# Performance work log

Measured on AMD Instinct MI355X. Metric: run time of the kernel, lower is better.

## Reference

```python
import jax, jax.numpy as jnp
import numpy as np

N = 32768
D = 512          # query_dim = key_dim = value_dim
H = 8            # num_heads


def setup_inputs() -> dict:
    key = jax.random.key(0)
    ks = jax.random.split(key, 8)
    s = 0.02
    return {
        "queries": jax.random.normal(ks[0], (N, D), dtype=jnp.float32),
        "keys": jax.random.normal(ks[1], (N, D), dtype=jnp.float32),
        "values": jax.random.normal(ks[2], (N, D), dtype=jnp.float32),
        # Linear weights stored as [in, out] (torch stores [out, in]; math identical)
        "Wq": jax.random.normal(ks[3], (D, D * H), dtype=jnp.float32) * s,
        "Wk": jax.random.normal(ks[4], (D, D * H), dtype=jnp.float32) * s,
        "Wv": jax.random.normal(ks[5], (D, D * H), dtype=jnp.float32) * s,
        "Wo": jax.random.normal(ks[6], (D * H, D), dtype=jnp.float32) * s,
        "bo": jax.random.normal(ks[7], (D,), dtype=jnp.float32) * s,
    }


def reference(queries, keys, values, Wq, Wk, Wv, Wo, bo):
    # Projections: [N, D] -> [N, H, D]
    Q = (queries @ Wq).reshape(-1, H, D)
    K = (keys @ Wk).reshape(-1, H, D)
    V = (values @ Wv).reshape(-1, H, D)
    # Per-token attention across the HEADS axis (faithful to torch.bmm on [N,H,D])
    attn = jnp.einsum("nhd,ngd->nhg", Q, K)      # [N, H, H], no 1/sqrt(d) scaling
    attn = jax.nn.softmax(attn, axis=-1)
    out = jnp.einsum("nhg,ngd->nhd", attn, V)    # [N, H, D]
    out = out.reshape(-1, H * D)
    return out @ Wo + bo                           # [N, D]
```

## Files before the change

### kernel.cpp

```cpp
#include <hip/hip_runtime.h>
#include <hip/hip_bf16.h>
#include <cstdint>


typedef unsigned short u16;
typedef unsigned int u32;
typedef __bf16 bf16x8 __attribute__((ext_vector_type(8)));
typedef float f32x4 __attribute__((ext_vector_type(4)));

#define DEVI __device__ __forceinline__

DEVI float b2f(u16 u) {
    union { u32 i; float f; } c; c.i = ((u32)u) << 16; return c.f;
}
DEVI u16 f2b(float f) {
    union { float f; u32 i; } c; c.f = f;
    return (u16)((c.i + 0x7FFFu + ((c.i >> 16) & 1u)) >> 16);
}
DEVI float asf(u32 x) { union { u32 i; float f; } c; c.i = x; return c.f; }

DEVI void async16(const u16* g, u16* l) {
    __builtin_amdgcn_global_load_lds(
        (const __attribute__((address_space(1))) u32*)g,
        (__attribute__((address_space(3))) u32*)l, 16, 0, 0);
}


__global__ __launch_bounds__(256) void cvt3_bf16(
    const float* __restrict__ a, const float* __restrict__ b,
    const float* __restrict__ c, u16* __restrict__ out, long ostride) {
    const float* in = (blockIdx.z == 0) ? a : (blockIdx.z == 1) ? b : c;
    u16* o = out + (long)blockIdx.z * ostride;
    const int i = blockIdx.x * 256 + threadIdx.x;
    const float4 x = ((const float4*)in)[2 * i];
    const float4 y = ((const float4*)in)[2 * i + 1];
    union { u16 u[8]; uint4 v; } r;
    r.u[0] = f2b(x.x); r.u[1] = f2b(x.y); r.u[2] = f2b(x.z); r.u[3] = f2b(x.w);
    r.u[4] = f2b(y.x); r.u[5] = f2b(y.y); r.u[6] = f2b(y.z); r.u[7] = f2b(y.w);
    ((uint4*)o)[i] = r.v;
}

__global__ void transpose_cvt(const float* __restrict__ in, u16* __restrict__ out,
                              int R, int C) {
    __shared__ float tile[32][33];
    const int c0 = blockIdx.x * 32, r0 = blockIdx.y * 32;
    const int x = threadIdx.x, y = threadIdx.y;
#pragma unroll
    for (int i = 0; i < 4; ++i) {
        const int r = y + i * 8;
        tile[x][r] = in[(long)(r0 + r) * C + c0 + x];
    }
    __syncthreads();
#pragma unroll
    for (int i = 0; i < 4; ++i) {
        const int c = y + i * 8;
        out[(long)(c0 + c) * R + r0 + x] = f2b(tile[c][x]);
    }
}


#define VM4 asm volatile("s_waitcnt vmcnt(4)" ::: "memory")
#define VM0 asm volatile("s_waitcnt vmcnt(0)" ::: "memory")
#define LGKM0 asm volatile("s_waitcnt lgkmcnt(0)" ::: "memory")
#define NOOP ((void)0)

#define STAGE_A(t, h)                                                     \
    do {                                                                  \
        const u16* _s = pA + (long)(h) * 128 * K + (long)(t) * 64;        \
        u16* _d = As + (((t) & 1) * 16384) + (h) * 8192 + wave * 512;     \
        async16(_s, _d);                                                  \
        async16(_s + 64 * (long)K, _d + 4096);                            \
    } while (0)

#define STAGE_B(t, h)                                                     \
    do {                                                                  \
        const u16* _s = pB + (long)(h) * 128 * K + (long)(t) * 64;        \
        u16* _d = Bs + (((t) & 1) * 16384) + (h) * 8192 + wave * 512;     \
        async16(_s, _d);                                                  \
        async16(_s + 64 * (long)K, _d + 4096);                            \
    } while (0)

#define PHASE(c, P, STG, VW)                                                   \
    {                                                                          \
        const u16* _sA = As + (c) * 16384;                                     \
        const u16* _sB = Bs + (c) * 16384;                                     \
        bf16x8 a00 = *(const bf16x8*)(_sA + arow_u + (2 * (P)) * 1024 + s0);   \
        bf16x8 a01 = *(const bf16x8*)(_sA + arow_u + (2 * (P)) * 1024 + s1);   \
        bf16x8 a10 = *(const bf16x8*)(_sA + arow_u + (2 * (P) + 1) * 1024 + s0); \
        bf16x8 a11 = *(const bf16x8*)(_sA + arow_u + (2 * (P) + 1) * 1024 + s1); \
        if ((P) == 0) {                                                        \
            _Pragma("unroll") for (int n = 0; n < 4; ++n) {                    \
                bfr[n][0] = *(const bf16x8*)(_sB + brow_u + n * 1024 + s0);    \
                bfr[n][1] = *(const bf16x8*)(_sB + brow_u + n * 1024 + s1);    \
            }                                                                  \
        }                                                                      \
        STG;                                                                   \
        __builtin_amdgcn_s_barrier();                                          \
        LGKM0;                                                                 \
        __builtin_amdgcn_s_setprio(1);                                         \
        _Pragma("unroll") for (int n = 0; n < 4; ++n) {                        \
            acc[2 * (P)][n] = __builtin_amdgcn_mfma_f32_16x16x32_bf16(         \
                a00, bfr[n][0], acc[2 * (P)][n], 0, 0, 0);                     \
            acc[2 * (P)][n] = __builtin_amdgcn_mfma_f32_16x16x32_bf16(         \
                a01, bfr[n][1], acc[2 * (P)][n], 0, 0, 0);                     \
            acc[2 * (P) + 1][n] = __builtin_amdgcn_mfma_f32_16x16x32_bf16(     \
                a10, bfr[n][0], acc[2 * (P) + 1][n], 0, 0, 0);                 \
            acc[2 * (P) + 1][n] = __builtin_amdgcn_mfma_f32_16x16x32_bf16(     \
                a11, bfr[n][1], acc[2 * (P) + 1][n], 0, 0, 0);                 \
        }                                                                      \
        __builtin_amdgcn_s_setprio(0);                                         \
        VW;                                                                    \
        __builtin_amdgcn_s_barrier();                                          \
    }

template <int F32OUT>
__global__ __launch_bounds__(512, 2) void gemm256(
    const u16* __restrict__ Ab, const u16* __restrict__ Bb,
    void* __restrict__ Cv, const float* __restrict__ bias,
    int M, int N, int K, long sAz, long sBz, long sCz) {
    __shared__ u16 As[2 * 16384];
    __shared__ u16 Bs[2 * 16384];
    (void)M;
    const int tid = threadIdx.x;
    const int wave = tid >> 6, lane = tid & 63;
    const int z = blockIdx.z;
    const u16* A = Ab + (long)z * sAz;
    const u16* BT = Bb + (long)z * sBz;

    int bx, by;
    {
        const int gx = gridDim.x, nwg = gx * gridDim.y;
        const int b = blockIdx.y * gx + blockIdx.x;
        if ((nwg & 7) == 0) {
            const int cpx = nwg >> 3;
            const int w = (b & 7) * cpx + (b >> 3);
            bx = w % gx; by = w / gx;
        } else { bx = blockIdx.x; by = blockIdx.y; }
    }
    const long row0 = (long)by * 256, col0 = (long)bx * 256;

    const int mrow = lane & 15, quad = lane >> 4;
    const int wr = wave >> 2, wc = wave & 3;
    const int s0 = ((quad ^ (mrow & 7)) << 3);
    const int s1 = (((4 | quad) ^ (mrow & 7)) << 3);
    const int arow_u = (wr * 128 + mrow) * 64;
    const int brow_u = (wc * 64 + mrow) * 64;

    const int sr = tid >> 3;
    const int skg = ((tid & 7) ^ (sr & 7)) << 3;
    const u16* pA = A + (row0 + sr) * (long)K + skg;
    const u16* pB = BT + (col0 + sr) * (long)K + skg;

    f32x4 acc[8][4] = {};
    bf16x8 bfr[4][2];

    const int NT = K >> 6;
    const int NI = NT >> 1;

    STAGE_A(0, 0); STAGE_A(0, 1); STAGE_B(0, 0); STAGE_B(0, 1);
    STAGE_B(1, 0); STAGE_B(1, 1);
    VM4;
    __builtin_amdgcn_s_barrier();

#pragma unroll 1
    for (int it = 0; it < NI - 1; ++it) {
        const int t1 = 2 * it + 1;
        PHASE(0, 0, STAGE_A(t1, 0), NOOP);
        PHASE(0, 1, STAGE_A(t1, 1), NOOP);
        PHASE(0, 2, STAGE_B(t1 + 1, 0), NOOP);
        PHASE(0, 3, STAGE_B(t1 + 1, 1), VM4);
        PHASE(1, 0, STAGE_A(t1 + 1, 0), NOOP);
        PHASE(1, 1, STAGE_A(t1 + 1, 1), NOOP);
        PHASE(1, 2, STAGE_B(t1 + 2, 0), NOOP);
        PHASE(1, 3, STAGE_B(t1 + 2, 1), VM4);
    }
    {
        const int tl = NT - 1;
        PHASE(0, 0, STAGE_A(tl, 0), NOOP);
        PHASE(0, 1, STAGE_A(tl, 1), NOOP);
        PHASE(0, 2, NOOP, NOOP);
        PHASE(0, 3, NOOP, VM0);
        PHASE(1, 0, NOOP, NOOP);
        PHASE(1, 1, NOOP, NOOP);
        PHASE(1, 2, NOOP, NOOP);
        PHASE(1, 3, NOOP, NOOP);
    }

    const long wrow = row0 + wr * 128;
    const long wcol = col0 + wc * 64;
    if (F32OUT) {
        float* C = (float*)Cv + (long)z * sCz;
        float bv[4];
#pragma unroll
        for (int n = 0; n < 4; ++n) bv[n] = bias[wcol + n * 16 + mrow];
#pragma unroll
        for (int m = 0; m < 8; ++m) {
            const long r = wrow + m * 16 + quad * 4;
#pragma unroll
            for (int n = 0; n < 4; ++n) {
                const long c = wcol + n * 16 + mrow;
#pragma unroll
                for (int rr = 0; rr < 4; ++rr)
                    C[(r + rr) * (long)N + c] = acc[m][n][rr] + bv[n];
            }
        }
    } else {
        u16* C = (u16*)Cv + (long)z * sCz;
#pragma unroll
        for (int m = 0; m < 8; ++m) {
            const long r = wrow + m * 16 + quad * 4;
#pragma unroll
            for (int n = 0; n < 4; ++n) {
                const long c = wcol + n * 16 + mrow;
#pragma unroll
                for (int rr = 0; rr < 4; ++rr)
                    C[(r + rr) * (long)N + c] = f2b(acc[m][n][rr]);
            }
        }
    }
}

#undef PHASE
#undef STAGE_A
#undef STAGE_B


DEVI float dot8(uint4 a, uint4 b) {
    const u32* pa = (const u32*)&a;
    const u32* pb = (const u32*)&b;
    float s = 0.f;
#pragma unroll
    for (int w = 0; w < 4; ++w) {
        s = fmaf(asf(pa[w] << 16), asf(pb[w] << 16), s);
        s = fmaf(asf(pa[w] & 0xFFFF0000u), asf(pb[w] & 0xFFFF0000u), s);
    }
    return s;
}

DEVI void acc8(float* o, uint4 v, float p) {
    const u32* pv = (const u32*)&v;
#pragma unroll
    for (int w = 0; w < 4; ++w) {
        o[2 * w]     = fmaf(p, asf(pv[w] << 16), o[2 * w]);
        o[2 * w + 1] = fmaf(p, asf(pv[w] & 0xFFFF0000u), o[2 * w + 1]);
    }
}

__global__ __launch_bounds__(256) void attn_kernel(
    const u16* __restrict__ Qg, const u16* __restrict__ Kg,
    const u16* __restrict__ Vg, u16* __restrict__ Og) {
    __shared__ uint4 sQ[8 * 65];
    __shared__ uint4 sK[8 * 65];
    __shared__ uint4 sV[512];
    __shared__ float part[4][64];
    __shared__ float logitS[64];
    __shared__ float probS[64];
    const int t = threadIdx.x;
    const long base = (long)blockIdx.x * 4096;

    const uint4* q4 = (const uint4*)(Qg + base);
    const uint4* k4 = (const uint4*)(Kg + base);
    const uint4* v4 = (const uint4*)(Vg + base);
    {
        const int r0 = t >> 6, c0 = t & 63;
        sQ[r0 * 65 + c0] = q4[t];
        sK[r0 * 65 + c0] = k4[t];
        const int r1 = r0 + 4;
        sQ[r1 * 65 + c0] = q4[t + 256];
        sK[r1 * 65 + c0] = k4[t + 256];
        sV[t] = v4[t];
        sV[t + 256] = v4[t + 256];
    }
    __syncthreads();

    {
        const int pr = t & 63, ch = t >> 6;
        const int h = pr >> 3, g = pr & 7;
        const uint4* qp = sQ + h * 65 + ch * 16;
        const uint4* kp = sK + g * 65 + ch * 16;
        float s = 0.f;
#pragma unroll
        for (int i = 0; i < 16; ++i) s += dot8(qp[i], kp[i]);
        part[ch][pr] = s;
    }
    __syncthreads();
    if (t < 64) logitS[t] = part[0][t] + part[1][t] + part[2][t] + part[3][t];
    __syncthreads();
    if (t < 8) {
        float m = logitS[t * 8];
#pragma unroll
        for (int g = 1; g < 8; ++g) m = fmaxf(m, logitS[t * 8 + g]);
        float e[8], sum = 0.f;
#pragma unroll
        for (int g = 0; g < 8; ++g) { e[g] = __expf(logitS[t * 8 + g] - m); sum += e[g]; }
        const float inv = 1.f / sum;
#pragma unroll
        for (int g = 0; g < 8; ++g) probS[t * 8 + g] = e[g] * inv;
    }
    __syncthreads();

    const int hh = t >> 5, c = t & 31;
    float p[8];
#pragma unroll
    for (int g = 0; g < 8; ++g) p[g] = probS[hh * 8 + g];
    float o0[8], o1[8];
#pragma unroll
    for (int j = 0; j < 8; ++j) { o0[j] = 0.f; o1[j] = 0.f; }
#pragma unroll
    for (int g = 0; g < 8; ++g) {
        const uint4 va = sV[g * 64 + c];
        const uint4 vb = sV[g * 64 + 32 + c];
        acc8(o0, va, p[g]);
        acc8(o1, vb, p[g]);
    }
    union { u16 u[8]; uint4 v; } ob;
#pragma unroll
    for (int j = 0; j < 8; ++j) ob.u[j] = f2b(o0[j]);
    *(uint4*)(Og + base + hh * 512 + c * 8) = ob.v;
#pragma unroll
    for (int j = 0; j < 8; ++j) ob.u[j] = f2b(o1[j]);
    *(uint4*)(Og + base + hh * 512 + 256 + c * 8) = ob.v;
}


extern "C" void kernel_launch(void* const* d_in, const int* in_sizes, int n_in,
                              void* d_out, int out_size, void* d_ws, size_t ws_size,
                              hipStream_t stream) {
    const float* Xq = (const float*)d_in[0];
    const float* Xk = (const float*)d_in[1];
    const float* Xv = (const float*)d_in[2];
    const float* Wq = (const float*)d_in[3];
    const float* Wk = (const float*)d_in[4];
    const float* Wv = (const float*)d_in[5];
    const float* Wo = (const float*)d_in[6];
    const float* bo = (const float*)d_in[7];

    const int N = 32768;
    const size_t W = 16777216ull;
    const size_t AO = 268435456ull;

    int McA = 0;
    for (int m = 8192; m >= 1024; m >>= 1)
        if (W + AO + (size_t)m * 27648ull <= ws_size) { McA = m; break; }

    char* ws = (char*)d_ws;
    u16* WqT = (u16*)(ws);
    u16* WoT = (u16*)(ws + 12582912ull);

    dim3 tb(32, 8);
    transpose_cvt<<<dim3(128, 16), tb, 0, stream>>>(Wq, WqT, 512, 4096);
    transpose_cvt<<<dim3(128, 16), tb, 0, stream>>>(Wk, WqT + 2097152, 512, 4096);
    transpose_cvt<<<dim3(128, 16), tb, 0, stream>>>(Wv, WqT + 4194304, 512, 4096);
    transpose_cvt<<<dim3(16, 128), tb, 0, stream>>>(Wo, WoT, 4096, 512);

    if (McA) {
        const int Mc = McA;
        u16* Ao  = (u16*)(ws + W);
        u16* Xb  = (u16*)(ws + W + AO);
        u16* Qc  = Xb + (size_t)3 * Mc * 512;
        u16* Kc  = Qc + (size_t)Mc * 4096;
        u16* Vc  = Kc + (size_t)Mc * 4096;
        const dim3 gProj(16, Mc / 256, 3);
        for (int m0 = 0; m0 < N; m0 += Mc) {
            const long xoff = (long)m0 * 512;
            cvt3_bf16<<<dim3(Mc / 4, 1, 3), 256, 0, stream>>>(
                Xq + xoff, Xk + xoff, Xv + xoff, Xb, (long)Mc * 512);
            gemm256<0><<<gProj, 512, 0, stream>>>(Xb, WqT, Qc, nullptr,
                                                  Mc, 4096, 512,
                                                  (long)Mc * 512, 2097152L,
                                                  (long)Mc * 4096);
            attn_kernel<<<Mc, 256, 0, stream>>>(Qc, Kc, Vc, Ao + (long)m0 * 4096);
        }
        gemm256<1><<<dim3(2, 128, 1), 512, 0, stream>>>(
            Ao, WoT, d_out, bo, N, 512, 4096, 0L, 0L, 0L);
    } else {
        int Mc = 8192;
        while (Mc > 256 && W + (size_t)Mc * 27648ull > ws_size) Mc >>= 1;
        if (W + (size_t)Mc * 27648ull > ws_size) return;
        u16* Xb = (u16*)(ws + W);
        u16* Qc = Xb + (size_t)3 * Mc * 512;
        u16* Kc = Qc + (size_t)Mc * 4096;
        u16* Vc = Kc + (size_t)Mc * 4096;
        const dim3 gProj(16, Mc / 256, 3);
        const dim3 gOut(2, Mc / 256, 1);
        for (int m0 = 0; m0 < N; m0 += Mc) {
            const long xoff = (long)m0 * 512;
            cvt3_bf16<<<dim3(Mc / 4, 1, 3), 256, 0, stream>>>(
                Xq + xoff, Xk + xoff, Xv + xoff, Xb, (long)Mc * 512);
            gemm256<0><<<gProj, 512, 0, stream>>>(Xb, WqT, Qc, nullptr,
                                                  Mc, 4096, 512,
                                                  (long)Mc * 512, 2097152L,
                                                  (long)Mc * 4096);
            attn_kernel<<<Mc, 256, 0, stream>>>(Qc, Kc, Vc, Qc);
            gemm256<1><<<gOut, 512, 0, stream>>>(Qc, WoT, (float*)d_out + xoff, bo,
                                                 Mc, 512, 4096, 0L, 0L, 0L);
        }
    }
}
```

Measured before the change: 1.353 ms.

## Make projection GEMM persistent over six output tiles with cross-tile prefetch

The QKV projection GEMM launches 8×(Mc/256) workgroups instead of 16×(Mc/256)×3. Each workgroup now loops over 6 output tiles, covering three matrices and two column halves. During the tail of each tile's K-loop it prefetches the first K-slices of the next tile, so the pipeline prologue and epilogue bubbles overlap with compute. The cost is a 6× smaller grid, which may leave CUs underoccupied or unbalanced. It also adds extra address arithmetic and a serialized epilogue store per tile.

```diff
diff --git a/kernel.cpp b/kernel.cpp
--- a/kernel.cpp
+++ b/kernel.cpp
@@ -64,17 +64,19 @@
 #define LGKM0 asm volatile("s_waitcnt lgkmcnt(0)" ::: "memory")
 #define NOOP ((void)0)
 
-#define STAGE_A(t, h)                                                     \
+#define STAGE_A(t, h, off)                                                \
     do {                                                                  \
-        const u16* _s = pA + (long)(h) * 128 * K + (long)(t) * 64;        \
+        const u16* _s = Ab + (off) + laneOff + (long)(h) * 128 * K +      \
+                        (long)(t) * 64;                                   \
         u16* _d = As + (((t) & 1) * 16384) + (h) * 8192 + wave * 512;     \
         async16(_s, _d);                                                  \
         async16(_s + 64 * (long)K, _d + 4096);                            \
     } while (0)
 
-#define STAGE_B(t, h)                                                     \
+#define STAGE_B(t, h, off)                                                \
     do {                                                                  \
-        const u16* _s = pB + (long)(h) * 128 * K + (long)(t) * 64;        \
+        const u16* _s = Bb + (off) + laneOff + (long)(h) * 128 * K +      \
+                        (long)(t) * 64;                                   \
         u16* _d = Bs + (((t) & 1) * 16384) + (h) * 8192 + wave * 512;     \
         async16(_s, _d);                                                  \
         async16(_s + 64 * (long)K, _d + 4096);                            \
@@ -113,7 +115,7 @@
         __builtin_amdgcn_s_barrier();                                          \
     }
 
-template <int F32OUT>
+template <int F32OUT, int MODE>
 __global__ __launch_bounds__(512, 2) void gemm256(
     const u16* __restrict__ Ab, const u16* __restrict__ Bb,
     void* __restrict__ Cv, const float* __restrict__ bias,
@@ -123,21 +125,23 @@
     (void)M;
     const int tid = threadIdx.x;
     const int wave = tid >> 6, lane = tid & 63;
-    const int z = blockIdx.z;
-    const u16* A = Ab + (long)z * sAz;
-    const u16* BT = Bb + (long)z * sBz;
-
-    int bx, by;
-    {
+
+    int b0, by;
+    long zoffA = 0, zoffB = 0, zoffC = 0;
+    if (MODE == 0) {
         const int gx = gridDim.x, nwg = gx * gridDim.y;
         const int b = blockIdx.y * gx + blockIdx.x;
         if ((nwg & 7) == 0) {
             const int cpx = nwg >> 3;
             const int w = (b & 7) * cpx + (b >> 3);
-            bx = w % gx; by = w / gx;
-        } else { bx = blockIdx.x; by = blockIdx.y; }
-    }
-    const long row0 = (long)by * 256, col0 = (long)bx * 256;
+            b0 = w % gx; by = w / gx;
+        } else { b0 = blockIdx.x; by = blockIdx.y; }
+        const int z = blockIdx.z;
+        zoffA = (long)z * sAz; zoffB = (long)z * sBz; zoffC = (long)z * sCz;
+    } else {
+        b0 = blockIdx.x; by = blockIdx.y;
+    }
+    const long row0 = (long)by * 256;
 
     const int mrow = lane & 15, quad = lane >> 4;
     const int wr = wave >> 2, wc = wave & 3;
@@ -148,76 +152,113 @@
 
     const int sr = tid >> 3;
     const int skg = ((tid & 7) ^ (sr & 7)) << 3;
-    const u16* pA = A + (row0 + sr) * (long)K + skg;
-    const u16* pB = BT + (col0 + sr) * (long)K + skg;
+    const long laneOff = (long)sr * K + skg;
 
     f32x4 acc[8][4] = {};
     bf16x8 bfr[4][2];
 
+    const int NC = (MODE == 1) ? 6 : 1;
     const int NT = K >> 6;
     const int NI = NT >> 1;
 
-    STAGE_A(0, 0); STAGE_A(0, 1); STAGE_B(0, 0); STAGE_B(0, 1);
-    STAGE_B(1, 0); STAGE_B(1, 1);
+    long oA, oB, colj, oA2, oB2, colj2;
+    {
+        if (MODE == 1) {
+            colj = (long)b0 * 256;
+            oA = row0 * (long)K;
+            oB = colj * (long)K;
+        } else {
+            colj = (long)b0 * 256;
+            oA = zoffA + row0 * (long)K;
+            oB = zoffB + colj * (long)K;
+        }
+    }
+
+    STAGE_A(0, 0, oA); STAGE_A(0, 1, oA);
+    STAGE_B(0, 0, oB); STAGE_B(0, 1, oB);
+    STAGE_B(1, 0, oB); STAGE_B(1, 1, oB);
     VM4;
     __builtin_amdgcn_s_barrier();
 
 #pragma unroll 1
-    for (int it = 0; it < NI - 1; ++it) {
-        const int t1 = 2 * it + 1;
-        PHASE(0, 0, STAGE_A(t1, 0), NOOP);
-        PHASE(0, 1, STAGE_A(t1, 1), NOOP);
-        PHASE(0, 2, STAGE_B(t1 + 1, 0), NOOP);
-        PHASE(0, 3, STAGE_B(t1 + 1, 1), VM4);
-        PHASE(1, 0, STAGE_A(t1 + 1, 0), NOOP);
-        PHASE(1, 1, STAGE_A(t1 + 1, 1), NOOP);
-        PHASE(1, 2, STAGE_B(t1 + 2, 0), NOOP);
-        PHASE(1, 3, STAGE_B(t1 + 2, 1), VM4);
-    }
-    {
-        const int tl = NT - 1;
-        PHASE(0, 0, STAGE_A(tl, 0), NOOP);
-        PHASE(0, 1, STAGE_A(tl, 1), NOOP);
-        PHASE(0, 2, NOOP, NOOP);
-        PHASE(0, 3, NOOP, VM0);
-        PHASE(1, 0, NOOP, NOOP);
-        PHASE(1, 1, NOOP, NOOP);
-        PHASE(1, 2, NOOP, NOOP);
-        PHASE(1, 3, NOOP, NOOP);
-    }
-
-    const long wrow = row0 + wr * 128;
-    const long wcol = col0 + wc * 64;
-    if (F32OUT) {
-        float* C = (float*)Cv + (long)z * sCz;
-        float bv[4];
-#pragma unroll
-        for (int n = 0; n < 4; ++n) bv[n] = bias[wcol + n * 16 + mrow];
-#pragma unroll
-        for (int m = 0; m < 8; ++m) {
-            const long r = wrow + m * 16 + quad * 4;
-#pragma unroll
-            for (int n = 0; n < 4; ++n) {
-                const long c = wcol + n * 16 + mrow;
-#pragma unroll
-                for (int rr = 0; rr < 4; ++rr)
-                    C[(r + rr) * (long)N + c] = acc[m][n][rr] + bv[n];
+    for (int j = 0; j < NC; ++j) {
+        {
+            const int jn = (j + 1 < NC) ? j + 1 : j;
+            if (MODE == 1) {
+                const int zn = jn >> 1;
+                colj2 = (long)(b0 + ((jn & 1) << 3)) * 256;
+                oA2 = (long)zn * sAz + row0 * (long)K;
+                oB2 = (long)zn * sBz + colj2 * (long)K;
+            } else { oA2 = oA; oB2 = oB; colj2 = colj; }
+        }
+#pragma unroll 1
+        for (int it = 0; it < NI - 1; ++it) {
+            const int t1 = 2 * it + 1;
+            PHASE(0, 0, STAGE_A(t1, 0, oA), NOOP);
+            PHASE(0, 1, STAGE_A(t1, 1, oA), NOOP);
+            PHASE(0, 2, STAGE_B(t1 + 1, 0, oB), NOOP);
+            PHASE(0, 3, STAGE_B(t1 + 1, 1, oB), VM4);
+            PHASE(1, 0, STAGE_A(t1 + 1, 0, oA), NOOP);
+            PHASE(1, 1, STAGE_A(t1 + 1, 1, oA), NOOP);
+            PHASE(1, 2, STAGE_B(t1 + 2, 0, oB), NOOP);
+            PHASE(1, 3, STAGE_B(t1 + 2, 1, oB), VM4);
+        }
+        {
+            PHASE(0, 0, STAGE_A(NT - 1, 0, oA), NOOP);
+            PHASE(0, 1, STAGE_A(NT - 1, 1, oA), NOOP);
+            PHASE(0, 2, STAGE_B(0, 0, oB2), NOOP);
+            PHASE(0, 3, STAGE_B(0, 1, oB2), VM4);
+            PHASE(1, 0, STAGE_A(0, 0, oA2), NOOP);
+            PHASE(1, 1, STAGE_A(0, 1, oA2), NOOP);
+            PHASE(1, 2, STAGE_B(1, 0, oB2), NOOP);
+            PHASE(1, 3, STAGE_B(1, 1, oB2), VM4);
+        }
+
+        {
+            const long wrow = row0 + wr * 128;
+            const long wcol = colj + wc * 64;
+            const long cz = (MODE == 1) ? (long)(j >> 1) * sCz : zoffC;
+            if (F32OUT) {
+                float* C = (float*)Cv + cz;
+                float bv[4];
+#pragma unroll
+                for (int n = 0; n < 4; ++n) bv[n] = bias[wcol + n * 16 + mrow];
+#pragma unroll
+                for (int m = 0; m < 8; ++m) {
+                    const long r = wrow + m * 16 + quad * 4;
+#pragma unroll
+                    for (int n = 0; n < 4; ++n) {
+                        const long c = wcol + n * 16 + mrow;
+#pragma unroll
+                        for (int rr = 0; rr < 4; ++rr)
+                            C[(r + rr) * (long)N + c] = acc[m][n][rr] + bv[n];
+                    }
+                }
+            } else {
+                u16* C = (u16*)Cv + cz;
+#pragma unroll
+                for (int m = 0; m < 8; ++m) {
+                    const long r = wrow + m * 16 + quad * 4;
+#pragma unroll
+                    for (int n = 0; n < 4; ++n) {
+                        const long c = wcol + n * 16 + mrow;
+#pragma unroll
+                        for (int rr = 0; rr < 4; ++rr)
+                            C[(r + rr) * (long)N + c] = f2b(acc[m][n][rr]);
+                    }
+                }
             }
-        }
-    } else {
-        u16* C = (u16*)Cv + (long)z * sCz;
-#pragma unroll
-        for (int m = 0; m < 8; ++m) {
-            const long r = wrow + m * 16 + quad * 4;
-#pragma unroll
-            for (int n = 0; n < 4; ++n) {
-                const long c = wcol + n * 16 + mrow;
-#pragma unroll
-                for (int rr = 0; rr < 4; ++rr)
-                    C[(r + rr) * (long)N + c] = f2b(acc[m][n][rr]);
+            if (j + 1 < NC) {
+#pragma unroll
+                for (int m = 0; m < 8; ++m)
+#pragma unroll
+                    for (int n = 0; n < 4; ++n)
+                        acc[m][n] = (f32x4){0.f, 0.f, 0.f, 0.f};
             }
         }
-    }
+        oA = oA2; oB = oB2; colj = colj2;
+    }
+    VM0;
 }
 
 #undef PHASE
@@ -360,18 +401,18 @@
         u16* Qc  = Xb + (size_t)3 * Mc * 512;
         u16* Kc  = Qc + (size_t)Mc * 4096;
         u16* Vc  = Kc + (size_t)Mc * 4096;
-        const dim3 gProj(16, Mc / 256, 3);
+        const dim3 gProj(8, Mc / 256, 1);
         for (int m0 = 0; m0 < N; m0 += Mc) {
             const long xoff = (long)m0 * 512;
             cvt3_bf16<<<dim3(Mc / 4, 1, 3), 256, 0, stream>>>(
                 Xq + xoff, Xk + xoff, Xv + xoff, Xb, (long)Mc * 512);
-            gemm256<0><<<gProj, 512, 0, stream>>>(Xb, WqT, Qc, nullptr,
-                                                  Mc, 4096, 512,
-                                                  (long)Mc * 512, 2097152L,
-                                                  (long)Mc * 4096);
+            gemm256<0, 1><<<gProj, 512, 0, stream>>>(Xb, WqT, Qc, nullptr,
+                                                     Mc, 4096, 512,
+                                                     (long)Mc * 512, 2097152L,
+                                                     (long)Mc * 4096);
             attn_kernel<<<Mc, 256, 0, stream>>>(Qc, Kc, Vc, Ao + (long)m0 * 4096);
         }
-        gemm256<1><<<dim3(2, 128, 1), 512, 0, stream>>>(
+        gemm256<1, 0><<<dim3(2, 128, 1), 512, 0, stream>>>(
             Ao, WoT, d_out, bo, N, 512, 4096, 0L, 0L, 0L);
     } else {
         int Mc = 8192;
@@ -381,19 +422,19 @@
         u16* Qc = Xb + (size_t)3 * Mc * 512;
         u16* Kc = Qc + (size_t)Mc * 4096;
         u16* Vc = Kc + (size_t)Mc * 4096;
-        const dim3 gProj(16, Mc / 256, 3);
+        const dim3 gProj(8, Mc / 256, 1);
         const dim3 gOut(2, Mc / 256, 1);
         for (int m0 = 0; m0 < N; m0 += Mc) {
             const long xoff = (long)m0 * 512;
             cvt3_bf16<<<dim3(Mc / 4, 1, 3), 256, 0, stream>>>(
                 Xq + xoff, Xk + xoff, Xv + xoff, Xb, (long)Mc * 512);
-            gemm256<0><<<gProj, 512, 0, stream>>>(Xb, WqT, Qc, nullptr,
-                                                  Mc, 4096, 512,
-                                                  (long)Mc * 512, 2097152L,
-                                                  (long)Mc * 4096);
+            gemm256<0, 1><<<gProj, 512, 0, stream>>>(Xb, WqT, Qc, nullptr,
+                                                     Mc, 4096, 512,
+                                                     (long)Mc * 512, 2097152L,
+                                                     (long)Mc * 4096);
             attn_kernel<<<Mc, 256, 0, stream>>>(Qc, Kc, Vc, Qc);
-            gemm256<1><<<gOut, 512, 0, stream>>>(Qc, WoT, (float*)d_out + xoff, bo,
-                                                 Mc, 512, 4096, 0L, 0L, 0L);
-        }
-    }
-}
+            gemm256<1, 0><<<gOut, 512, 0, stream>>>(Qc, WoT, (float*)d_out + xoff, bo,
+                                                    Mc, 512, 4096, 0L, 0L, 0L);
+        }
+    }
+}
```

Measured after the change: 1.410 ms. +4.2%, slower.
